# Optimization experiments

Hardware: AMD Instinct MI355X
Metric: run time of the kernel (lower is better)

## Reference

```python
import jax, jax.numpy as jnp
import numpy as np

IN_F, OUT_F, NG = 2048, 8192, 16
EPS = 1e-5

def setup_inputs() -> dict:
    key = jax.random.key(0)
    k = jax.random.split(key, 6)
    x = jax.random.normal(k[0], (4096, IN_F), dtype=jnp.float32)
    W = jax.random.normal(k[1], (OUT_F, IN_F), dtype=jnp.float32) * (1.0 / np.sqrt(IN_F))
    b = jax.random.normal(k[2], (OUT_F,), dtype=jnp.float32) * 0.01
    gn_w = jnp.ones((OUT_F,), dtype=jnp.float32)
    gn_b = jnp.zeros((OUT_F,), dtype=jnp.float32)
    mult_w = jax.random.normal(k[3], (OUT_F,), dtype=jnp.float32)
    return {"x": x, "W": W, "b": b, "gn_w": gn_w, "gn_b": gn_b, "mult_w": mult_w}

def reference(x, W, b, gn_w, gn_b, mult_w):
    B = x.shape[0]
    y = x @ W.T + b  # [B, OUT_F]
    g = y.reshape(B, NG, OUT_F // NG)
    mean = jnp.mean(g, axis=-1, keepdims=True)
    var = jnp.mean(jnp.square(g - mean), axis=-1, keepdims=True)
    n = ((g - mean) * jax.lax.rsqrt(var + EPS)).reshape(B, OUT_F)
    n = n * gn_w + gn_b
    s1 = n * jax.nn.sigmoid(n)
    m = s1 * mult_w
    return m * jax.nn.sigmoid(m)
```

## Files before the change

kernel.cpp:

```cpp
#include <hip/hip_runtime.h>

#define M_DIM 4096
#define N_DIM 8192
#define K_DIM 2048
#define NGRP 16
#define GSZ 512
#define EPSV 1e-5f

#define NX (M_DIM * K_DIM)
#define NW (N_DIM * K_DIM)
#define NY ((size_t)M_DIM * N_DIM)

typedef __attribute__((ext_vector_type(8))) short bf16x8;
typedef __attribute__((ext_vector_type(4))) float f32x4;
typedef __attribute__((ext_vector_type(8))) short shortx8;

__device__ __forceinline__ float b2f(short u) {
    union { unsigned u32; float f; } c;
    c.u32 = ((unsigned)(unsigned short)u) << 16;
    return c.f;
}

__device__ __forceinline__ short f2b(float f) {
    union { float f; unsigned u; } c; c.f = f;
    unsigned r = (c.u + 0x7fffu + ((c.u >> 16) & 1u)) >> 16;
    return (short)r;
}

__global__ __launch_bounds__(256) void convert_kernel(
    const float* __restrict__ x, const float* __restrict__ W,
    short* __restrict__ dst)
{
    const size_t base = ((size_t)blockIdx.x * 256 + threadIdx.x) * 32;
    const float* src = (base < NX) ? (x + base) : (W + (base - NX));
    f32x4 v[8];
#pragma unroll
    for (int c = 0; c < 8; ++c) v[c] = *(const f32x4*)(src + c * 4);
#pragma unroll
    for (int c = 0; c < 4; ++c) {
        shortx8 o;
#pragma unroll
        for (int j = 0; j < 4; ++j) {
            o[j]     = f2b(v[2 * c][j]);
            o[j + 4] = f2b(v[2 * c + 1][j]);
        }
        *(shortx8*)(dst + base + c * 8) = o;
    }
}

#define BKS 32
#define NTILES (K_DIM / BKS)

__global__ __launch_bounds__(512, 2) void gemm256_bf16_kernel(
    const short* __restrict__ A, const short* __restrict__ W, short* __restrict__ C)
{
    __shared__ __align__(16) short lds[4 * 16384];

    const int tid  = threadIdx.x;
    const int lane = tid & 63;
    const int wave = tid >> 6;
    const int wr   = wave >> 2;
    const int wc   = wave & 3;
    const int blockRow = blockIdx.y * 256;
    const int blockCol = blockIdx.x * 256;

    const int q0 = tid, q1 = tid + 512;
    const int sr0 = q0 >> 2, sc0 = (q0 & 3) ^ ((q0 >> 3) & 3);
    const int sr1 = q1 >> 2, sc1 = (q1 & 3) ^ ((q1 >> 3) & 3);
    const int offA0 = (blockRow + sr0) * K_DIM + sc0 * 8;
    const int offA1 = (blockRow + sr1) * K_DIM + sc1 * 8;
    const int offB0 = (blockCol + sr0) * K_DIM + sc0 * 8;
    const int offB1 = (blockCol + sr1) * K_DIM + sc1 * 8;

    const int fr    = lane & 15;
    const int pbyte = ((lane >> 4) ^ ((fr >> 1) & 3)) * 16;
    const int aBase = (wr * 128 + fr) * 64 + pbyte;
    const int bBase = (wc * 64  + fr) * 64 + pbyte;

    f32x4 acc[8][4] = {};

    auto stageT = [&](int t) {
        short* dA = lds + (t & 3) * 16384;
        short* dB = dA + 8192;
        const int ko = t * BKS;
        __builtin_amdgcn_global_load_lds(
            (const __attribute__((address_space(1))) void*)(A + offA0 + ko),
            (__attribute__((address_space(3))) void*)(dA + q0 * 8), 16, 0, 0);
        __builtin_amdgcn_global_load_lds(
            (const __attribute__((address_space(1))) void*)(W + offB0 + ko),
            (__attribute__((address_space(3))) void*)(dB + q0 * 8), 16, 0, 0);
        __builtin_amdgcn_global_load_lds(
            (const __attribute__((address_space(1))) void*)(A + offA1 + ko),
            (__attribute__((address_space(3))) void*)(dA + q1 * 8), 16, 0, 0);
        __builtin_amdgcn_global_load_lds(
            (const __attribute__((address_space(1))) void*)(W + offB1 + ko),
            (__attribute__((address_space(3))) void*)(dB + q1 * 8), 16, 0, 0);
    };

    auto ldfrags = [&](int t, bf16x8 (&f)[12]) {
        const char* bufA = (const char*)lds + (t & 3) * 32768;
        const char* bufB = bufA + 16384;
#pragma unroll
        for (int i = 0; i < 8; ++i)
            f[i] = *(const bf16x8*)(bufA + aBase + i * 1024);
#pragma unroll
        for (int j = 0; j < 4; ++j)
            f[8 + j] = *(const bf16x8*)(bufB + bBase + j * 1024);
    };

    auto domfma = [&](bf16x8 (&f)[12]) {
        __builtin_amdgcn_s_setprio(1);
#pragma unroll
        for (int i = 0; i < 8; ++i)
#pragma unroll
            for (int j = 0; j < 4; ++j)
                acc[i][j] = __builtin_amdgcn_mfma_f32_16x16x32_bf16(
                    f[i], f[8 + j], acc[i][j], 0, 0, 0);
        __builtin_amdgcn_s_setprio(0);
    };

    auto step = [&](int t, bf16x8 (&cur)[12], bf16x8 (&nxt)[12]) {
        if (t + 3 < NTILES) {
            stageT(t + 3);
            asm volatile("s_waitcnt vmcnt(8)" ::: "memory");
        } else if (t + 2 < NTILES) {
            asm volatile("s_waitcnt vmcnt(4)" ::: "memory");
        } else if (t + 1 < NTILES) {
            asm volatile("s_waitcnt vmcnt(0)" ::: "memory");
        }
        __builtin_amdgcn_s_barrier();
        __builtin_amdgcn_sched_barrier(0);
        if (t + 1 < NTILES) {
            ldfrags(t + 1, nxt);
            asm volatile("s_waitcnt lgkmcnt(12)" ::: "memory");
        } else {
            asm volatile("s_waitcnt lgkmcnt(0)" ::: "memory");
        }
        __builtin_amdgcn_sched_barrier(0);
        __builtin_amdgcn_s_barrier();
        __builtin_amdgcn_sched_barrier(0);
        domfma(cur);
    };

    bf16x8 fE[12], fO[12];

    stageT(0); stageT(1); stageT(2);
    asm volatile("s_waitcnt vmcnt(8)" ::: "memory");
    __builtin_amdgcn_s_barrier();
    __builtin_amdgcn_sched_barrier(0);
    ldfrags(0, fE);

    for (int t = 0; t < NTILES; t += 2) {
        step(t,     fE, fO);
        step(t + 1, fO, fE);
    }

    const int er = (lane >> 4) * 4;
    const int ec = lane & 15;
#pragma unroll
    for (int i = 0; i < 8; ++i) {
        const int rr = blockRow + wr * 128 + i * 16 + er;
#pragma unroll
        for (int j = 0; j < 4; ++j) {
            const int cc = blockCol + wc * 64 + j * 16 + ec;
#pragma unroll
            for (int r = 0; r < 4; ++r)
                C[(size_t)(rr + r) * N_DIM + cc] = f2b(acc[i][j][r]);
        }
    }
}

__global__ __launch_bounds__(256) void gn_silu_bf16_kernel(
    const short* __restrict__ Y,
    const float* __restrict__ bias,
    const float* __restrict__ gnw,
    const float* __restrict__ gnb,
    const float* __restrict__ mw,
    float* __restrict__ out)
{
    const int lane = threadIdx.x & 63;
    const int wave = threadIdx.x >> 6;
    const unsigned gid = blockIdx.x * 4u + wave;
    const unsigned row = gid >> 4;
    const unsigned grp = gid & 15;
    const int col = grp * GSZ + lane * 8;
    const size_t off = (size_t)row * N_DIM + col;

    bf16x8 v = *(const bf16x8*)(Y + off);
    f32x4 b0 = *(const f32x4*)(bias + col);
    f32x4 b1 = *(const f32x4*)(bias + col + 4);

    float y[8];
    float s = 0.f, s2 = 0.f;
#pragma unroll
    for (int j = 0; j < 8; ++j) {
        y[j] = b2f(v[j]) + (j < 4 ? b0[j] : b1[j - 4]);
        s  += y[j];
        s2 += y[j] * y[j];
    }
#pragma unroll
    for (int d = 1; d < 64; d <<= 1) {
        s  += __shfl_xor(s,  d, 64);
        s2 += __shfl_xor(s2, d, 64);
    }
    const float mean = s * (1.0f / GSZ);
    const float var  = s2 * (1.0f / GSZ) - mean * mean;
    const float inv  = rsqrtf(var + EPSV);

    f32x4 w0 = *(const f32x4*)(gnw + col);
    f32x4 w1 = *(const f32x4*)(gnw + col + 4);
    f32x4 g0 = *(const f32x4*)(gnb + col);
    f32x4 g1 = *(const f32x4*)(gnb + col + 4);
    f32x4 m0 = *(const f32x4*)(mw + col);
    f32x4 m1 = *(const f32x4*)(mw + col + 4);

    f32x4 o0, o1;
#pragma unroll
    for (int j = 0; j < 8; ++j) {
        float gwv = j < 4 ? w0[j] : w1[j - 4];
        float gbv = j < 4 ? g0[j] : g1[j - 4];
        float mwv = j < 4 ? m0[j] : m1[j - 4];
        float n  = (y[j] - mean) * inv * gwv + gbv;
        float s1 = n / (1.f + __expf(-n));
        float m  = s1 * mwv;
        float r  = m / (1.f + __expf(-m));
        if (j < 4) o0[j] = r; else o1[j - 4] = r;
    }
    *(f32x4*)(out + off)     = o0;
    *(f32x4*)(out + off + 4) = o1;
}

__global__ __launch_bounds__(256) void gemm_bt_f32_kernel(
    const float* __restrict__ A, const float* __restrict__ W, float* __restrict__ C)
{
    __shared__ __align__(16) short ldsA[128 * 32];
    __shared__ __align__(16) short ldsB[128 * 32];

    const int tid  = threadIdx.x;
    const int lane = tid & 63;
    const int wave = tid >> 6;
    const int blockRow = blockIdx.y * 128;
    const int blockCol = blockIdx.x * 128;
    const int srow = tid >> 1;
    const int scol = (tid & 1) * 16;
    const int wm  = (wave >> 1) * 64;
    const int wn  = (wave & 1) * 64;
    const int fr  = lane & 15;
    const int fko = (lane >> 4) * 8;

    f32x4 acc[4][4] = {};
    const size_t aRowOff = (size_t)(blockRow + srow) * K_DIM;
    const size_t wRowOff = (size_t)(blockCol + srow) * K_DIM;

    for (int k0 = 0; k0 < K_DIM; k0 += 32) {
        f32x4 va0 = *(const f32x4*)(A + aRowOff + k0 + scol);
        f32x4 va1 = *(const f32x4*)(A + aRowOff + k0 + scol + 4);
        f32x4 va2 = *(const f32x4*)(A + aRowOff + k0 + scol + 8);
        f32x4 va3 = *(const f32x4*)(A + aRowOff + k0 + scol + 12);
        f32x4 vb0 = *(const f32x4*)(W + wRowOff + k0 + scol);
        f32x4 vb1 = *(const f32x4*)(W + wRowOff + k0 + scol + 4);
        f32x4 vb2 = *(const f32x4*)(W + wRowOff + k0 + scol + 8);
        f32x4 vb3 = *(const f32x4*)(W + wRowOff + k0 + scol + 12);
        bf16x8 a0, a1, b0, b1;
#pragma unroll
        for (int j = 0; j < 4; ++j) {
            a0[j] = f2b(va0[j]); a0[j + 4] = f2b(va1[j]);
            a1[j] = f2b(va2[j]); a1[j + 4] = f2b(va3[j]);
            b0[j] = f2b(vb0[j]); b0[j + 4] = f2b(vb1[j]);
            b1[j] = f2b(vb2[j]); b1[j + 4] = f2b(vb3[j]);
        }
        *(bf16x8*)(ldsA + srow * 32 + scol)     = a0;
        *(bf16x8*)(ldsA + srow * 32 + scol + 8) = a1;
        *(bf16x8*)(ldsB + srow * 32 + scol)     = b0;
        *(bf16x8*)(ldsB + srow * 32 + scol + 8) = b1;
        __syncthreads();

        bf16x8 af[4], bfv[4];
#pragma unroll
        for (int i = 0; i < 4; ++i) {
            af[i]  = *(const bf16x8*)(ldsA + (wm + i * 16 + fr) * 32 + fko);
            bfv[i] = *(const bf16x8*)(ldsB + (wn + i * 16 + fr) * 32 + fko);
        }
#pragma unroll
        for (int i = 0; i < 4; ++i)
#pragma unroll
            for (int j = 0; j < 4; ++j)
                acc[i][j] = __builtin_amdgcn_mfma_f32_16x16x32_bf16(
                    af[i], bfv[j], acc[i][j], 0, 0, 0);
        __syncthreads();
    }

    const int er = (lane >> 4) * 4;
    const int ec = lane & 15;
#pragma unroll
    for (int i = 0; i < 4; ++i) {
        const int r0 = blockRow + wm + i * 16 + er;
#pragma unroll
        for (int j = 0; j < 4; ++j) {
            const int c0 = blockCol + wn + j * 16 + ec;
#pragma unroll
            for (int r = 0; r < 4; ++r)
                C[(size_t)(r0 + r) * N_DIM + c0] = acc[i][j][r];
        }
    }
}

__global__ __launch_bounds__(256) void gn_silu_f32_kernel(
    float* __restrict__ Y,
    const float* __restrict__ bias,
    const float* __restrict__ gnw,
    const float* __restrict__ gnb,
    const float* __restrict__ mw)
{
    const int lane = threadIdx.x & 63;
    const int wave = threadIdx.x >> 6;
    const unsigned gid = blockIdx.x * 4u + wave;
    const unsigned row = gid >> 4;
    const unsigned grp = gid & 15;
    const int col = grp * GSZ + lane * 8;
    const size_t off = (size_t)row * N_DIM + col;

    f32x4 v0 = *(const f32x4*)(Y + off);
    f32x4 v1 = *(const f32x4*)(Y + off + 4);
    f32x4 b0 = *(const f32x4*)(bias + col);
    f32x4 b1 = *(const f32x4*)(bias + col + 4);

    float y[8];
    float s = 0.f, s2 = 0.f;
#pragma unroll
    for (int j = 0; j < 8; ++j) {
        y[j] = (j < 4 ? v0[j] + b0[j] : v1[j - 4] + b1[j - 4]);
        s += y[j]; s2 += y[j] * y[j];
    }
#pragma unroll
    for (int d = 1; d < 64; d <<= 1) {
        s  += __shfl_xor(s,  d, 64);
        s2 += __shfl_xor(s2, d, 64);
    }
    const float mean = s * (1.0f / GSZ);
    const float var  = s2 * (1.0f / GSZ) - mean * mean;
    const float inv  = rsqrtf(var + EPSV);

    f32x4 w0 = *(const f32x4*)(gnw + col);
    f32x4 w1 = *(const f32x4*)(gnw + col + 4);
    f32x4 g0 = *(const f32x4*)(gnb + col);
    f32x4 g1 = *(const f32x4*)(gnb + col + 4);
    f32x4 m0 = *(const f32x4*)(mw + col);
    f32x4 m1 = *(const f32x4*)(mw + col + 4);

    f32x4 o0, o1;
#pragma unroll
    for (int j = 0; j < 8; ++j) {
        float gwv = j < 4 ? w0[j] : w1[j - 4];
        float gbv = j < 4 ? g0[j] : g1[j - 4];
        float mwv = j < 4 ? m0[j] : m1[j - 4];
        float n  = (y[j] - mean) * inv * gwv + gbv;
        float s1 = n / (1.f + __expf(-n));
        float m  = s1 * mwv;
        float r  = m / (1.f + __expf(-m));
        if (j < 4) o0[j] = r; else o1[j - 4] = r;
    }
    *(f32x4*)(Y + off)     = o0;
    *(f32x4*)(Y + off + 4) = o1;
}

extern "C" void kernel_launch(void* const* d_in, const int* in_sizes, int n_in,
                              void* d_out, int out_size, void* d_ws, size_t ws_size,
                              hipStream_t stream)
{
    const float* x   = (const float*)d_in[0];
    const float* W   = (const float*)d_in[1];
    const float* b   = (const float*)d_in[2];
    const float* gnw = (const float*)d_in[3];
    const float* gnb = (const float*)d_in[4];
    const float* mw  = (const float*)d_in[5];
    float* out = (float*)d_out;

    const size_t need = ((size_t)NX + NW + NY) * sizeof(short);
    const int ngroups = M_DIM * NGRP;

    if (ws_size >= need) {
        short* xb = (short*)d_ws;
        short* Wb = xb + NX;
        short* yb = Wb + NW;

        convert_kernel<<<(NX + NW) / (256 * 32), 256, 0, stream>>>(x, W, xb);
        dim3 g256(N_DIM / 256, M_DIM / 256);
        gemm256_bf16_kernel<<<g256, 512, 0, stream>>>(xb, Wb, yb);
        gn_silu_bf16_kernel<<<ngroups / 4, 256, 0, stream>>>(yb, b, gnw, gnb, mw, out);
    } else {
        dim3 ggrid(N_DIM / 128, M_DIM / 128);
        gemm_bt_f32_kernel<<<ggrid, 256, 0, stream>>>(x, W, out);
        gn_silu_f32_kernel<<<ngroups / 4, 256, 0, stream>>>(out, b, gnw, gnb, mw);
    }
}
```

Before: 369.8 us.

## Simplify GEMM to double-buffered LDS, raise occupancy, swizzle block order

Replaces the 4-stage LDS ring with register-fragment double buffering by a simpler 2-stage LDS double buffer. Fragments are now loaded and consumed within the same iteration, under an extra barrier. This halves LDS use and raises the launch-bounds occupancy hint from 2 to 4 blocks. It also swaps the 2D grid for a 1D grid with a block-index swizzle, so that consecutive blocks go to different XCDs and share L2 reuse. The cost is less overlap between LDS fragment loads and MFMA, and the higher occupancy hint may force register spilling with 128 accumulator floats per thread.

```diff
diff --git a/kernel.cpp b/kernel.cpp
--- a/kernel.cpp
+++ b/kernel.cpp
@@ -51,18 +51,21 @@
 #define BKS 32
 #define NTILES (K_DIM / BKS)
 
-__global__ __launch_bounds__(512, 2) void gemm256_bf16_kernel(
+__global__ __launch_bounds__(512, 4) void gemm256_bf16_kernel(
     const short* __restrict__ A, const short* __restrict__ W, short* __restrict__ C)
 {
-    __shared__ __align__(16) short lds[4 * 16384];
+    __shared__ __align__(16) short lds[2 * 16384];
 
     const int tid  = threadIdx.x;
     const int lane = tid & 63;
     const int wave = tid >> 6;
     const int wr   = wave >> 2;
     const int wc   = wave & 3;
-    const int blockRow = blockIdx.y * 256;
-    const int blockCol = blockIdx.x * 256;
+
+    const unsigned orig = blockIdx.x;
+    const unsigned swz  = (orig & 7) * 64 + (orig >> 3);
+    const int blockCol = (swz & 31) * 256;
+    const int blockRow = (swz >> 5) * 256;
 
     const int q0 = tid, q1 = tid + 512;
     const int sr0 = q0 >> 2, sc0 = (q0 & 3) ^ ((q0 >> 3) & 3);
@@ -80,7 +83,7 @@
     f32x4 acc[8][4] = {};
 
     auto stageT = [&](int t) {
-        short* dA = lds + (t & 3) * 16384;
+        short* dA = lds + (t & 1) * 16384;
         short* dB = dA + 8192;
         const int ko = t * BKS;
         __builtin_amdgcn_global_load_lds(
@@ -97,62 +100,41 @@
             (__attribute__((address_space(3))) void*)(dB + q1 * 8), 16, 0, 0);
     };
 
-    auto ldfrags = [&](int t, bf16x8 (&f)[12]) {
-        const char* bufA = (const char*)lds + (t & 3) * 32768;
-        const char* bufB = bufA + 16384;
-#pragma unroll
-        for (int i = 0; i < 8; ++i)
-            f[i] = *(const bf16x8*)(bufA + aBase + i * 1024);
-#pragma unroll
-        for (int j = 0; j < 4; ++j)
-            f[8 + j] = *(const bf16x8*)(bufB + bBase + j * 1024);
-    };
-
-    auto domfma = [&](bf16x8 (&f)[12]) {
-        __builtin_amdgcn_s_setprio(1);
-#pragma unroll
-        for (int i = 0; i < 8; ++i)
-#pragma unroll
-            for (int j = 0; j < 4; ++j)
-                acc[i][j] = __builtin_amdgcn_mfma_f32_16x16x32_bf16(
-                    f[i], f[8 + j], acc[i][j], 0, 0, 0);
-        __builtin_amdgcn_s_setprio(0);
-    };
-
-    auto step = [&](int t, bf16x8 (&cur)[12], bf16x8 (&nxt)[12]) {
-        if (t + 3 < NTILES) {
-            stageT(t + 3);
-            asm volatile("s_waitcnt vmcnt(8)" ::: "memory");
-        } else if (t + 2 < NTILES) {
+    stageT(0);
+
+    for (int t = 0; t < NTILES; ++t) {
+        if (t + 1 < NTILES) {
+            stageT(t + 1);
             asm volatile("s_waitcnt vmcnt(4)" ::: "memory");
-        } else if (t + 1 < NTILES) {
+        } else {
             asm volatile("s_waitcnt vmcnt(0)" ::: "memory");
-        }
-        __builtin_amdgcn_s_barrier();
-        __builtin_amdgcn_sched_barrier(0);
-        if (t + 1 < NTILES) {
-            ldfrags(t + 1, nxt);
-            asm volatile("s_waitcnt lgkmcnt(12)" ::: "memory");
-        } else {
-            asm volatile("s_waitcnt lgkmcnt(0)" ::: "memory");
         }
         __builtin_amdgcn_sched_barrier(0);
         __builtin_amdgcn_s_barrier();
         __builtin_amdgcn_sched_barrier(0);
-        domfma(cur);
-    };
-
-    bf16x8 fE[12], fO[12];
-
-    stageT(0); stageT(1); stageT(2);
-    asm volatile("s_waitcnt vmcnt(8)" ::: "memory");
-    __builtin_amdgcn_s_barrier();
-    __builtin_amdgcn_sched_barrier(0);
-    ldfrags(0, fE);
-
-    for (int t = 0; t < NTILES; t += 2) {
-        step(t,     fE, fO);
-        step(t + 1, fO, fE);
+
+        const char* bufA = (const char*)lds + (t & 1) * 32768;
+        const char* bufB = bufA + 16384;
+        bf16x8 af[8], bfv[4];
+#pragma unroll
+        for (int i = 0; i < 8; ++i)
+            af[i] = *(const bf16x8*)(bufA + aBase + i * 1024);
+#pragma unroll
+        for (int j = 0; j < 4; ++j)
+            bfv[j] = *(const bf16x8*)(bufB + bBase + j * 1024);
+        asm volatile("s_waitcnt lgkmcnt(0)" ::: "memory");
+        __builtin_amdgcn_sched_barrier(0);
+        __builtin_amdgcn_s_barrier();
+        __builtin_amdgcn_sched_barrier(0);
+
+        __builtin_amdgcn_s_setprio(1);
+#pragma unroll
+        for (int i = 0; i < 8; ++i)
+#pragma unroll
+            for (int j = 0; j < 4; ++j)
+                acc[i][j] = __builtin_amdgcn_mfma_f32_16x16x32_bf16(
+                    af[i], bfv[j], acc[i][j], 0, 0, 0);
+        __builtin_amdgcn_s_setprio(0);
     }
 
     const int er = (lane >> 4) * 4;
@@ -385,8 +367,7 @@
         short* yb = Wb + NW;
 
         convert_kernel<<<(NX + NW) / (256 * 32), 256, 0, stream>>>(x, W, xb);
-        dim3 g256(N_DIM / 256, M_DIM / 256);
-        gemm256_bf16_kernel<<<g256, 512, 0, stream>>>(xb, Wb, yb);
+        gemm256_bf16_kernel<<<512, 512, 0, stream>>>(xb, Wb, yb);
         gn_silu_bf16_kernel<<<ngroups / 4, 256, 0, stream>>>(yb, b, gnw, gnb, mw, out);
     } else {
         dim3 ggrid(N_DIM / 128, M_DIM / 128);
```

After: 1.473 ms. +298.5%, slower.

## Restructure GEMM main loop to one barrier per tile with asm LDS fragment reads

Applied to the files above, without the earlier changes.

The GEMM K-loop is reworked so that each iteration issues the global-to-LDS prefetch two tiles ahead instead of three, and uses a single workgroup barrier instead of two. The LDS fragment reads for the next tile are emitted as inline-asm ds_read_b128 with immediate offsets. They are waited on only at the start of the following iteration, so they can overlap with the current tile's MFMAs. The loop is fully specialized, with explicit tail iterations replacing the runtime NTILES checks. The aim is less barrier stalling and better overlap of LDS latency with matrix math. The trade-off is a shallower global prefetch and reliance on hand-managed waitcnts that the compiler cannot see.

```diff
diff --git a/kernel.cpp b/kernel.cpp
--- a/kernel.cpp
+++ b/kernel.cpp
@@ -13,6 +13,7 @@
 
 typedef __attribute__((ext_vector_type(8))) short bf16x8;
 typedef __attribute__((ext_vector_type(4))) float f32x4;
+typedef __attribute__((ext_vector_type(4))) int   i32x4;
 typedef __attribute__((ext_vector_type(8))) short shortx8;
 
 __device__ __forceinline__ float b2f(short u) {
@@ -78,82 +79,87 @@
     const int bBase = (wc * 64  + fr) * 64 + pbyte;
 
     f32x4 acc[8][4] = {};
-
-    auto stageT = [&](int t) {
+    i32x4 fA0[8], fB0[4], fA1[8], fB1[4];
+
+    auto gll = [&](const short* g, short* l) {
+        __builtin_amdgcn_global_load_lds(
+            (const __attribute__((address_space(1))) void*)g,
+            (__attribute__((address_space(3))) void*)l, 16, 0, 0);
+    };
+    auto stage4 = [&](int t) {
         short* dA = lds + (t & 3) * 16384;
         short* dB = dA + 8192;
         const int ko = t * BKS;
-        __builtin_amdgcn_global_load_lds(
-            (const __attribute__((address_space(1))) void*)(A + offA0 + ko),
-            (__attribute__((address_space(3))) void*)(dA + q0 * 8), 16, 0, 0);
-        __builtin_amdgcn_global_load_lds(
-            (const __attribute__((address_space(1))) void*)(W + offB0 + ko),
-            (__attribute__((address_space(3))) void*)(dB + q0 * 8), 16, 0, 0);
-        __builtin_amdgcn_global_load_lds(
-            (const __attribute__((address_space(1))) void*)(A + offA1 + ko),
-            (__attribute__((address_space(3))) void*)(dA + q1 * 8), 16, 0, 0);
-        __builtin_amdgcn_global_load_lds(
-            (const __attribute__((address_space(1))) void*)(W + offB1 + ko),
-            (__attribute__((address_space(3))) void*)(dB + q1 * 8), 16, 0, 0);
+        gll(A + offA0 + ko, dA + q0 * 8);
+        gll(W + offB0 + ko, dB + q0 * 8);
+        gll(A + offA1 + ko, dA + q1 * 8);
+        gll(W + offB1 + ko, dB + q1 * 8);
     };
 
-    auto ldfrags = [&](int t, bf16x8 (&f)[12]) {
-        const char* bufA = (const char*)lds + (t & 3) * 32768;
-        const char* bufB = bufA + 16384;
-#pragma unroll
-        for (int i = 0; i < 8; ++i)
-            f[i] = *(const bf16x8*)(bufA + aBase + i * 1024);
-#pragma unroll
-        for (int j = 0; j < 4; ++j)
-            f[8 + j] = *(const bf16x8*)(bufB + bBase + j * 1024);
+    auto ldfrags = [&](int t, i32x4 (&fa)[8], i32x4 (&fb)[4]) {
+        unsigned vA = (unsigned)(__UINTPTR_TYPE__)
+            (__attribute__((address_space(3))) short*)(lds + (t & 3) * 16384) + (unsigned)aBase;
+        unsigned vB = (unsigned)(__UINTPTR_TYPE__)
+            (__attribute__((address_space(3))) short*)(lds + (t & 3) * 16384 + 8192) + (unsigned)bBase;
+        asm volatile("ds_read_b128 %0, %1 offset:0"    : "=v"(fa[0]) : "v"(vA));
+        asm volatile("ds_read_b128 %0, %1 offset:1024" : "=v"(fa[1]) : "v"(vA));
+        asm volatile("ds_read_b128 %0, %1 offset:2048" : "=v"(fa[2]) : "v"(vA));
+        asm volatile("ds_read_b128 %0, %1 offset:3072" : "=v"(fa[3]) : "v"(vA));
+        asm volatile("ds_read_b128 %0, %1 offset:4096" : "=v"(fa[4]) : "v"(vA));
+        asm volatile("ds_read_b128 %0, %1 offset:5120" : "=v"(fa[5]) : "v"(vA));
+        asm volatile("ds_read_b128 %0, %1 offset:6144" : "=v"(fa[6]) : "v"(vA));
+        asm volatile("ds_read_b128 %0, %1 offset:7168" : "=v"(fa[7]) : "v"(vA));
+        asm volatile("ds_read_b128 %0, %1 offset:0"    : "=v"(fb[0]) : "v"(vB));
+        asm volatile("ds_read_b128 %0, %1 offset:1024" : "=v"(fb[1]) : "v"(vB));
+        asm volatile("ds_read_b128 %0, %1 offset:2048" : "=v"(fb[2]) : "v"(vB));
+        asm volatile("ds_read_b128 %0, %1 offset:3072" : "=v"(fb[3]) : "v"(vB));
     };
 
-    auto domfma = [&](bf16x8 (&f)[12]) {
+    auto domfma = [&](i32x4 (&fa)[8], i32x4 (&fb)[4]) {
         __builtin_amdgcn_s_setprio(1);
 #pragma unroll
         for (int i = 0; i < 8; ++i)
 #pragma unroll
             for (int j = 0; j < 4; ++j)
                 acc[i][j] = __builtin_amdgcn_mfma_f32_16x16x32_bf16(
-                    f[i], f[8 + j], acc[i][j], 0, 0, 0);
+                    __builtin_bit_cast(bf16x8, fa[i]),
+                    __builtin_bit_cast(bf16x8, fb[j]),
+                    acc[i][j], 0, 0, 0);
         __builtin_amdgcn_s_setprio(0);
     };
 
-    auto step = [&](int t, bf16x8 (&cur)[12], bf16x8 (&nxt)[12]) {
-        if (t + 3 < NTILES) {
-            stageT(t + 3);
-            asm volatile("s_waitcnt vmcnt(8)" ::: "memory");
-        } else if (t + 2 < NTILES) {
+    auto iter = [&](int t, i32x4 (&ca)[8], i32x4 (&cb)[4],
+                    i32x4 (&na)[8], i32x4 (&nb)[4], int mode) {
+        if (mode == 0) {
+            stage4(t + 2);
             asm volatile("s_waitcnt vmcnt(4)" ::: "memory");
-        } else if (t + 1 < NTILES) {
+        } else if (mode == 1) {
             asm volatile("s_waitcnt vmcnt(0)" ::: "memory");
         }
-        __builtin_amdgcn_s_barrier();
+        asm volatile("s_waitcnt lgkmcnt(0)" ::: "memory");
         __builtin_amdgcn_sched_barrier(0);
-        if (t + 1 < NTILES) {
-            ldfrags(t + 1, nxt);
-            asm volatile("s_waitcnt lgkmcnt(12)" ::: "memory");
-        } else {
-            asm volatile("s_waitcnt lgkmcnt(0)" ::: "memory");
-        }
-        __builtin_amdgcn_sched_barrier(0);
-        __builtin_amdgcn_s_barrier();
-        __builtin_amdgcn_sched_barrier(0);
-        domfma(cur);
+        if (mode != 2) {
+            __builtin_amdgcn_s_barrier();
+            __builtin_amdgcn_sched_barrier(0);
+            ldfrags(t + 1, na, nb);
+            __builtin_amdgcn_sched_barrier(0);
+        }
+        domfma(ca, cb);
     };
 
-    bf16x8 fE[12], fO[12];
-
-    stageT(0); stageT(1); stageT(2);
-    asm volatile("s_waitcnt vmcnt(8)" ::: "memory");
+    stage4(0); stage4(1);
+    asm volatile("s_waitcnt vmcnt(4)" ::: "memory");
     __builtin_amdgcn_s_barrier();
     __builtin_amdgcn_sched_barrier(0);
-    ldfrags(0, fE);
-
-    for (int t = 0; t < NTILES; t += 2) {
-        step(t,     fE, fO);
-        step(t + 1, fO, fE);
-    }
+    ldfrags(0, fA0, fB0);
+    __builtin_amdgcn_sched_barrier(0);
+
+    for (int t = 0; t < 62; t += 2) {
+        iter(t,     fA0, fB0, fA1, fB1, 0);
+        iter(t + 1, fA1, fB1, fA0, fB0, 0);
+    }
+    iter(62, fA0, fB0, fA1, fB1, 1);
+    iter(63, fA1, fB1, fA0, fB0, 2);
 
     const int er = (lane >> 4) * 4;
     const int ec = lane & 15;
```

After: 365.5 us. No clear change (-1.1%).
